# Kernel optimization log

Hardware: AMD Instinct MI355X
Metric: run time of the kernel (lower is better)

## Reference

```python
import jax, jax.numpy as jnp
import numpy as np
from jax import lax

H = 106      # hidden size
IN = 100     # input feature size
S = 512      # sequence length (time-major)
B = 256      # batch
N_REST = 10  # layers 2..6 of lstm1 (5) + all 5 layers of lstm2, all 106->106


def _lstm_layer(x, Wih, Whh, bih, bhh):
    """Single LSTM layer, PyTorch gate order (i, f, g, o). x: (S, B, in)."""
    # Precompute input contribution for all timesteps at once: (S, B, 4H)
    gx = jnp.einsum('sbi,gi->sbg', x, Wih) + bih + bhh

    def step(carry, g_t):
        h, c = carry
        g = g_t + h @ Whh.T                      # (B, 4H)
        i, f, gg, o = jnp.split(g, 4, axis=-1)
        i = jax.nn.sigmoid(i)
        f = jax.nn.sigmoid(f)
        gg = jnp.tanh(gg)
        o = jax.nn.sigmoid(o)
        c = f * c + i * gg
        h = o * jnp.tanh(c)
        return (h, c), h

    b = x.shape[1]
    h0 = jnp.zeros((b, H), x.dtype)
    c0 = jnp.zeros((b, H), x.dtype)
    _, ys = lax.scan(step, (h0, c0), gx)
    return ys  # (S, B, H)


def setup_inputs() -> dict:
    key = jax.random.key(0)
    ks = jax.random.split(key, 10)
    k = 1.0 / np.sqrt(H)  # PyTorch LSTM default uniform init bound
    u = lambda kk, shape: jax.random.uniform(kk, shape, jnp.float32, -k, k)

    noise = jax.random.normal(ks[0], (S, B, IN), jnp.float32)
    # First layer: input dim 100
    W_ih0 = u(ks[1], (4 * H, IN))
    W_hh0 = u(ks[2], (4 * H, H))
    b_ih0 = u(ks[3], (4 * H,))
    b_hh0 = u(ks[4], (4 * H,))
    # Remaining 10 layers: input dim 106, stacked
    W_ih = u(ks[5], (N_REST, 4 * H, H))
    W_hh = u(ks[6], (N_REST, 4 * H, H))
    b_ih = u(ks[7], (N_REST, 4 * H))
    b_hh = u(ks[8], (N_REST, 4 * H))
    return {"noise": noise, "W_ih0": W_ih0, "W_hh0": W_hh0, "b_ih0": b_ih0,
            "b_hh0": b_hh0, "W_ih": W_ih, "W_hh": W_hh, "b_ih": b_ih, "b_hh": b_hh}


def reference(noise, W_ih0, W_hh0, b_ih0, b_hh0, W_ih, W_hh, b_ih, b_hh):
    x = _lstm_layer(noise, W_ih0, W_hh0, b_ih0, b_hh0)

    def layer_step(xc, params):
        Wih, Whh, bih, bhh = params
        return _lstm_layer(xc, Wih, Whh, bih, bhh), None

    x, _ = lax.scan(layer_step, x, (W_ih, W_hh, b_ih, b_hh))
    return x  # (S, B, H)
```

## Files before the change

### kernel.cpp

```cpp
#include <hip/hip_runtime.h>
#include <cmath>


namespace {
constexpr int H = 106, G4 = 424, SEQ = 512, BB = 256, KIN0 = 100;
constexpr int GST = 436;
constexpr int NTHR = 896;
constexpr int RGN = 16;
constexpr int NLAYER = 11;
constexpr int RD = 16;
constexpr int REL = 56;
constexpr int KMAC = 8;
constexpr size_t CNT_STRIDE = 16;
constexpr size_t RING_OFF_B = 65536;
constexpr size_t RING_PER_L = (size_t)RD * BB * REL;

using f16x8 = __attribute__((ext_vector_type(8))) _Float16;
using f32x4 = __attribute__((ext_vector_type(4))) float;
typedef unsigned long long u64;

__device__ __forceinline__ u64 ald(const u64* p) {
    return __hip_atomic_load(p, __ATOMIC_RELAXED, __HIP_MEMORY_SCOPE_AGENT);
}
__device__ __forceinline__ void ast(u64* p, u64 v) {
    __hip_atomic_store(p, v, __ATOMIC_RELAXED, __HIP_MEMORY_SCOPE_AGENT);
}
__device__ __forceinline__ unsigned aldu(const unsigned* p) {
    return __hip_atomic_load(p, __ATOMIC_RELAXED, __HIP_MEMORY_SCOPE_AGENT);
}
__device__ __forceinline__ void astu(unsigned* p, unsigned v) {
    __hip_atomic_store(p, v, __ATOMIC_RELAXED, __HIP_MEMORY_SCOPE_AGENT);
}
__device__ __forceinline__ void spinc(const unsigned* p, unsigned tgt) {
    while (aldu(p) < tgt) __builtin_amdgcn_s_sleep(8);
}
__device__ __forceinline__ float fast_tanh(float x) {
    float t = __expf(2.0f * x);
    return 1.0f - 2.0f / (t + 1.0f);
}
__device__ __forceinline__ float act_gate(float g, bool istanh) {
    float s = istanh ? 2.0f * g : g;
    float r = 1.0f / (1.0f + __expf(-s));
    return istanh ? 2.0f * r - 1.0f : r;
}
__device__ __forceinline__ unsigned packh2(float a, float b) {
    unsigned lo = (unsigned)__builtin_bit_cast(unsigned short, (_Float16)a);
    unsigned hi = (unsigned)__builtin_bit_cast(unsigned short, (_Float16)b);
    return (hi << 16) | lo;
}

__global__ __launch_bounds__(NTHR)
__attribute__((amdgpu_waves_per_eu(4, 4)))
void lstm_wave(const float* __restrict__ noise,
               float* __restrict__ yout,
               unsigned* cnt, u64* ring,
               const float* __restrict__ W_ih0, const float* __restrict__ W_hh0,
               const float* __restrict__ b_ih0, const float* __restrict__ b_hh0,
               const float* __restrict__ W_ih,  const float* __restrict__ W_hh,
               const float* __restrict__ b_ih,  const float* __restrict__ b_hh)
{
    const int l = blockIdx.x / RGN;
    const int rg = blockIdx.x % RGN;
    const bool LAST = (l == NLAYER - 1);
    const int K_IN = (l == 0) ? KIN0 : H;

    const float* Wih = (l == 0) ? W_ih0 : W_ih + (size_t)(l - 1) * G4 * H;
    const float* Whh = (l == 0) ? W_hh0 : W_hh + (size_t)(l - 1) * G4 * H;
    const float* pbi = (l == 0) ? b_ih0 : b_ih + (size_t)(l - 1) * G4;
    const float* pbh = (l == 0) ? b_hh0 : b_hh + (size_t)(l - 1) * G4;

    unsigned* cons_my = cnt + (size_t)(l * RGN + rg) * CNT_STRIDE;
    unsigned* cons_in = cnt + (size_t)((l - 1) * RGN + rg) * CNT_STRIDE;
    u64* ring_in  = ring + (size_t)(l - 1) * RING_PER_L;
    u64* ring_out = ring + (size_t)l * RING_PER_L;

    __shared__ __align__(16) _Float16 sx[KMAC][16 * 136];
    __shared__ __align__(16) _Float16 sh[16 * 136];
    __shared__ float gl[16 * GST];

    const int tid = threadIdx.x;
    const int w = tid >> 6, lane = tid & 63;
    const int l16 = lane & 15, kg = lane >> 4;
    const int lm = tid / 56, ld = tid % 56;
    const int um = tid / 53, up = tid % 53;

    f16x8 bf[2][8];
    float bias[2];
    #pragma unroll
    for (int t = 0; t < 2; ++t) {
        const int n = 16 * (2 * w + t) + l16;
        const bool valid = n < G4;
        const float* pwx = Wih + (size_t)(valid ? n : 0) * K_IN;
        const float* pwh = Whh + (size_t)(valid ? n : 0) * H;
        #pragma unroll
        for (int q = 0; q < 8; ++q) {
            f16x8 v;
            #pragma unroll
            for (int e = 0; e < 8; ++e) {
                const int k = 32 * q + 8 * kg + e;
                float f = 0.0f;
                if (valid) {
                    if (k < 128) { if (k < K_IN) f = pwx[k]; }
                    else { const int kh = k - 128; if (kh < H) f = pwh[kh]; }
                }
                v[e] = (_Float16)f;
            }
            bf[t][q] = v;
        }
        bias[t] = valid ? (pbi[n] + pbh[n]) : 0.0f;
    }

    for (int i = tid; i < KMAC * 1088 + 1088; i += NTHR) {
        if (i < KMAC * 1088) ((unsigned*)sx)[i] = 0;
        else ((unsigned*)sh)[i - KMAC * 1088] = 0;
    }
    float c0 = 0.0f, c1 = 0.0f;
    __syncthreads();

    for (int m = 0; m < SEQ / KMAC; ++m) {
        unsigned xw[KMAC] = {0, 0, 0, 0, 0, 0, 0, 0};
        if (l == 0) {
            if (ld < 50) {
                #pragma unroll
                for (int ss = 0; ss < KMAC; ++ss) {
                    const int s = KMAC * m + ss;
                    const float2 t = *(const float2*)(noise +
                        ((size_t)s * BB + rg * 16 + lm) * KIN0 + 2 * ld);
                    xw[ss] = packh2(t.x, t.y);
                }
            }
        } else {
            u64 v[KMAC];
            #pragma unroll
            for (int ss = 0; ss < KMAC; ++ss) {
                const int s = KMAC * m + ss;
                v[ss] = ald(ring_in + ((size_t)(s & (RD - 1)) * BB + rg * 16 + lm) * REL + ld);
            }
            #pragma unroll
            for (int ss = 0; ss < KMAC; ++ss) {
                const int s = KMAC * m + ss;
                const unsigned expt = (unsigned)(s + 1);
                const u64* pin = ring_in + ((size_t)(s & (RD - 1)) * BB + rg * 16 + lm) * REL + ld;
                u64 vv = v[ss];
                while ((unsigned)(vv >> 32) != expt) { __builtin_amdgcn_s_sleep(2); vv = ald(pin); }
                xw[ss] = (unsigned)vv;
            }
        }
        if (tid == 0 && !LAST && m >= 2) spinc(cons_my, (unsigned)(KMAC * m - 8));
        if (l > 0 || ld < 50) {
            #pragma unroll
            for (int ss = 0; ss < KMAC; ++ss)
                ((unsigned*)sx)[ss * 1088 + lm * 68 + ld] = xw[ss];
        }
        __syncthreads();
        if (tid == 0 && l > 0) astu(cons_in, (unsigned)(KMAC * m + KMAC));

        for (int ss = 0; ss < KMAC; ++ss) {
            const int s = KMAC * m + ss;
            f32x4 acc[2] = {{0, 0, 0, 0}, {0, 0, 0, 0}};
            const _Float16* ax = &sx[ss][l16 * 136 + 8 * kg];
            #pragma unroll
            for (int q = 0; q < 4; ++q) {
                const f16x8 a = *(const f16x8*)(ax + 32 * q);
                acc[0] = __builtin_amdgcn_mfma_f32_16x16x32_f16(a, bf[0][q], acc[0], 0, 0, 0);
                acc[1] = __builtin_amdgcn_mfma_f32_16x16x32_f16(a, bf[1][q], acc[1], 0, 0, 0);
            }
            const _Float16* ah = &sh[l16 * 136 + 8 * kg];
            #pragma unroll
            for (int q = 4; q < 8; ++q) {
                const f16x8 a = *(const f16x8*)(ah + 32 * (q - 4));
                acc[0] = __builtin_amdgcn_mfma_f32_16x16x32_f16(a, bf[0][q], acc[0], 0, 0, 0);
                acc[1] = __builtin_amdgcn_mfma_f32_16x16x32_f16(a, bf[1][q], acc[1], 0, 0, 0);
            }
            #pragma unroll
            for (int t = 0; t < 2; ++t) {
                const int n = 16 * (2 * w + t) + l16;
                if (n < G4) {
                    const bool istanh = (n >= 2 * H) && (n < 3 * H);
                    #pragma unroll
                    for (int r = 0; r < 4; ++r)
                        gl[(4 * kg + r) * GST + n] = act_gate(acc[t][r] + bias[t], istanh);
                }
            }
            __syncthreads();

            if (tid < 848) {
                const float* gm = gl + um * GST;
                const float2 vi = *(const float2*)(gm + 2 * up);
                const float2 vf = *(const float2*)(gm + H + 2 * up);
                const float2 vg = *(const float2*)(gm + 2 * H + 2 * up);
                const float2 vo = *(const float2*)(gm + 3 * H + 2 * up);
                c0 = fmaf(vf.x, c0, vi.x * vg.x);
                c1 = fmaf(vf.y, c1, vi.y * vg.y);
                const float h0 = vo.x * fast_tanh(c0);
                const float h1 = vo.y * fast_tanh(c1);
                const unsigned hw = packh2(h0, h1);
                ((unsigned*)sh)[um * 68 + up] = hw;
                if (LAST) {
                    *(float2*)(yout + ((size_t)s * BB + rg * 16 + um) * H + 2 * up) =
                        make_float2(h0, h1);
                } else {
                    ast(ring_out + ((size_t)(s & (RD - 1)) * BB + rg * 16 + um) * REL + up,
                        ((u64)(unsigned)(s + 1) << 32) | hw);
                }
            } else if (!LAST) {
                const int t2 = tid - 848, mm = t2 / 3, dd = t2 % 3;
                ast(ring_out + ((size_t)(s & (RD - 1)) * BB + rg * 16 + mm) * REL + 53 + dd,
                    (u64)(unsigned)(s + 1) << 32);
            }
            __syncthreads();
        }
    }
}
}

extern "C" void kernel_launch(void* const* d_in, const int* in_sizes, int n_in,
                              void* d_out, int out_size, void* d_ws, size_t ws_size,
                              hipStream_t stream) {
    const float* noise = (const float*)d_in[0];
    const float* W_ih0 = (const float*)d_in[1];
    const float* W_hh0 = (const float*)d_in[2];
    const float* b_ih0 = (const float*)d_in[3];
    const float* b_hh0 = (const float*)d_in[4];
    const float* W_ih  = (const float*)d_in[5];
    const float* W_hh  = (const float*)d_in[6];
    const float* b_ih  = (const float*)d_in[7];
    const float* b_hh  = (const float*)d_in[8];

    const size_t clear_bytes = RING_OFF_B + (size_t)10 * RING_PER_L * sizeof(u64);
    hipMemsetAsync(d_ws, 0, clear_bytes, stream);

    unsigned* cnt = (unsigned*)d_ws;
    u64* ring = (u64*)((char*)d_ws + RING_OFF_B);

    lstm_wave<<<dim3(NLAYER * RGN), dim3(NTHR), 0, stream>>>(
        noise, (float*)d_out, cnt, ring,
        W_ih0, W_hh0, b_ih0, b_hh0, W_ih, W_hh, b_ih, b_hh);
}
```

Baseline: 1.287 ms.

## Shrink block to 8 waves and precompute next step's input MFMA off critical path

The block drops from 14 to 8 waves, so each wave now owns 3-4 gate column tiles instead of 2, and the elementwise and load work is looped twice per thread. The input-projection MFMAs for the next timestep are issued right after the cell update, before the barrier, so only the recurrent half stays on the serial per-step path. Fewer waves should make barriers cheaper. In exchange, each wave does more serial MFMA and elementwise work, and register pressure rises from holding 4 weight tiles plus the precomputed accumulators.

```diff
diff --git a/kernel.cpp b/kernel.cpp
--- a/kernel.cpp
+++ b/kernel.cpp
@@ -4,8 +4,8 @@
 
 namespace {
 constexpr int H = 106, G4 = 424, SEQ = 512, BB = 256, KIN0 = 100;
-constexpr int GST = 436;
-constexpr int NTHR = 896;
+constexpr int GST = 434;
+constexpr int NTHR = 512;
 constexpr int RGN = 16;
 constexpr int NLAYER = 11;
 constexpr int RD = 16;
@@ -50,7 +50,7 @@
 }
 
 __global__ __launch_bounds__(NTHR)
-__attribute__((amdgpu_waves_per_eu(4, 4)))
+__attribute__((amdgpu_waves_per_eu(2, 2)))
 void lstm_wave(const float* __restrict__ noise,
                float* __restrict__ yout,
                unsigned* cnt, u64* ring,
@@ -76,20 +76,20 @@
 
     __shared__ __align__(16) _Float16 sx[KMAC][16 * 136];
     __shared__ __align__(16) _Float16 sh[16 * 136];
-    __shared__ float gl[16 * GST];
+    __shared__ __align__(16) float gl[16 * GST];
 
     const int tid = threadIdx.x;
     const int w = tid >> 6, lane = tid & 63;
     const int l16 = lane & 15, kg = lane >> 4;
-    const int lm = tid / 56, ld = tid % 56;
-    const int um = tid / 53, up = tid % 53;
-
-    f16x8 bf[2][8];
-    float bias[2];
+    const int NT = (w < 4) ? 4 : 3;
+    const int tb = (w < 4) ? 4 * w : 16 + 3 * (w - 4);
+
+    f16x8 bf[4][8];
+    float bias[4];
     #pragma unroll
-    for (int t = 0; t < 2; ++t) {
-        const int n = 16 * (2 * w + t) + l16;
-        const bool valid = n < G4;
+    for (int t = 0; t < 4; ++t) {
+        const int n = 16 * (tb + t) + l16;
+        const bool valid = (t < NT) && (n < G4);
         const float* pwx = Wih + (size_t)(valid ? n : 0) * K_IN;
         const float* pwh = Whh + (size_t)(valid ? n : 0) * H;
         #pragma unroll
@@ -114,68 +114,90 @@
         if (i < KMAC * 1088) ((unsigned*)sx)[i] = 0;
         else ((unsigned*)sh)[i - KMAC * 1088] = 0;
     }
-    float c0 = 0.0f, c1 = 0.0f;
+    float c0[2] = {0.f, 0.f}, c1[2] = {0.f, 0.f};
     __syncthreads();
 
+    f32x4 accx[4];
+
     for (int m = 0; m < SEQ / KMAC; ++m) {
-        unsigned xw[KMAC] = {0, 0, 0, 0, 0, 0, 0, 0};
-        if (l == 0) {
-            if (ld < 50) {
-                #pragma unroll
-                for (int ss = 0; ss < KMAC; ++ss) {
-                    const int s = KMAC * m + ss;
-                    const float2 t = *(const float2*)(noise +
-                        ((size_t)s * BB + rg * 16 + lm) * KIN0 + 2 * ld);
-                    xw[ss] = packh2(t.x, t.y);
-                }
-            }
-        } else {
-            u64 v[KMAC];
-            #pragma unroll
-            for (int ss = 0; ss < KMAC; ++ss) {
-                const int s = KMAC * m + ss;
-                v[ss] = ald(ring_in + ((size_t)(s & (RD - 1)) * BB + rg * 16 + lm) * REL + ld);
-            }
-            #pragma unroll
-            for (int ss = 0; ss < KMAC; ++ss) {
-                const int s = KMAC * m + ss;
-                const unsigned expt = (unsigned)(s + 1);
-                const u64* pin = ring_in + ((size_t)(s & (RD - 1)) * BB + rg * 16 + lm) * REL + ld;
-                u64 vv = v[ss];
-                while ((unsigned)(vv >> 32) != expt) { __builtin_amdgcn_s_sleep(2); vv = ald(pin); }
-                xw[ss] = (unsigned)vv;
+        #pragma unroll
+        for (int e = 0; e < 2; ++e) {
+            const int flat = tid + NTHR * e;
+            if (flat < 896) {
+                const int lm = flat / 56, ld = flat % 56;
+                unsigned xw[KMAC];
+                if (l == 0) {
+                    #pragma unroll
+                    for (int ss = 0; ss < KMAC; ++ss) {
+                        unsigned r = 0;
+                        if (ld < 50) {
+                            const int s = KMAC * m + ss;
+                            const float2 t = *(const float2*)(noise +
+                                ((size_t)s * BB + rg * 16 + lm) * KIN0 + 2 * ld);
+                            r = packh2(t.x, t.y);
+                        }
+                        xw[ss] = r;
+                    }
+                } else {
+                    u64 v[KMAC];
+                    #pragma unroll
+                    for (int ss = 0; ss < KMAC; ++ss) {
+                        const int s = KMAC * m + ss;
+                        v[ss] = ald(ring_in + ((size_t)(s & (RD - 1)) * BB + rg * 16 + lm) * REL + ld);
+                    }
+                    #pragma unroll
+                    for (int ss = 0; ss < KMAC; ++ss) {
+                        const int s = KMAC * m + ss;
+                        const unsigned expt = (unsigned)(s + 1);
+                        const u64* pin = ring_in + ((size_t)(s & (RD - 1)) * BB + rg * 16 + lm) * REL + ld;
+                        u64 vv = v[ss];
+                        while ((unsigned)(vv >> 32) != expt) { __builtin_amdgcn_s_sleep(2); vv = ald(pin); }
+                        xw[ss] = (unsigned)vv;
+                    }
+                }
+                if (l > 0 || ld < 50) {
+                    #pragma unroll
+                    for (int ss = 0; ss < KMAC; ++ss)
+                        ((unsigned*)sx)[ss * 1088 + lm * 68 + ld] = xw[ss];
+                }
             }
         }
         if (tid == 0 && !LAST && m >= 2) spinc(cons_my, (unsigned)(KMAC * m - 8));
-        if (l > 0 || ld < 50) {
-            #pragma unroll
-            for (int ss = 0; ss < KMAC; ++ss)
-                ((unsigned*)sx)[ss * 1088 + lm * 68 + ld] = xw[ss];
-        }
         __syncthreads();
         if (tid == 0 && l > 0) astu(cons_in, (unsigned)(KMAC * m + KMAC));
 
+        {
+            #pragma unroll
+            for (int t = 0; t < 4; ++t) accx[t] = f32x4{0, 0, 0, 0};
+            const _Float16* ax = &sx[0][l16 * 136 + 8 * kg];
+            #pragma unroll
+            for (int q = 0; q < 4; ++q) {
+                const f16x8 a = *(const f16x8*)(ax + 32 * q);
+                #pragma unroll
+                for (int t = 0; t < 4; ++t)
+                    if (t < NT)
+                        accx[t] = __builtin_amdgcn_mfma_f32_16x16x32_f16(a, bf[t][q], accx[t], 0, 0, 0);
+            }
+        }
+
         for (int ss = 0; ss < KMAC; ++ss) {
             const int s = KMAC * m + ss;
-            f32x4 acc[2] = {{0, 0, 0, 0}, {0, 0, 0, 0}};
-            const _Float16* ax = &sx[ss][l16 * 136 + 8 * kg];
-            #pragma unroll
-            for (int q = 0; q < 4; ++q) {
-                const f16x8 a = *(const f16x8*)(ax + 32 * q);
-                acc[0] = __builtin_amdgcn_mfma_f32_16x16x32_f16(a, bf[0][q], acc[0], 0, 0, 0);
-                acc[1] = __builtin_amdgcn_mfma_f32_16x16x32_f16(a, bf[1][q], acc[1], 0, 0, 0);
-            }
+            f32x4 acc[4];
+            #pragma unroll
+            for (int t = 0; t < 4; ++t) acc[t] = accx[t];
             const _Float16* ah = &sh[l16 * 136 + 8 * kg];
             #pragma unroll
             for (int q = 4; q < 8; ++q) {
                 const f16x8 a = *(const f16x8*)(ah + 32 * (q - 4));
-                acc[0] = __builtin_amdgcn_mfma_f32_16x16x32_f16(a, bf[0][q], acc[0], 0, 0, 0);
-                acc[1] = __builtin_amdgcn_mfma_f32_16x16x32_f16(a, bf[1][q], acc[1], 0, 0, 0);
-            }
-            #pragma unroll
-            for (int t = 0; t < 2; ++t) {
-                const int n = 16 * (2 * w + t) + l16;
-                if (n < G4) {
+                #pragma unroll
+                for (int t = 0; t < 4; ++t)
+                    if (t < NT)
+                        acc[t] = __builtin_amdgcn_mfma_f32_16x16x32_f16(a, bf[t][q], acc[t], 0, 0, 0);
+            }
+            #pragma unroll
+            for (int t = 0; t < 4; ++t) {
+                const int n = 16 * (tb + t) + l16;
+                if (t < NT && n < G4) {
                     const bool istanh = (n >= 2 * H) && (n < 3 * H);
                     #pragma unroll
                     for (int r = 0; r < 4; ++r)
@@ -184,29 +206,47 @@
             }
             __syncthreads();
 
-            if (tid < 848) {
-                const float* gm = gl + um * GST;
-                const float2 vi = *(const float2*)(gm + 2 * up);
-                const float2 vf = *(const float2*)(gm + H + 2 * up);
-                const float2 vg = *(const float2*)(gm + 2 * H + 2 * up);
-                const float2 vo = *(const float2*)(gm + 3 * H + 2 * up);
-                c0 = fmaf(vf.x, c0, vi.x * vg.x);
-                c1 = fmaf(vf.y, c1, vi.y * vg.y);
-                const float h0 = vo.x * fast_tanh(c0);
-                const float h1 = vo.y * fast_tanh(c1);
-                const unsigned hw = packh2(h0, h1);
-                ((unsigned*)sh)[um * 68 + up] = hw;
-                if (LAST) {
-                    *(float2*)(yout + ((size_t)s * BB + rg * 16 + um) * H + 2 * up) =
-                        make_float2(h0, h1);
-                } else {
-                    ast(ring_out + ((size_t)(s & (RD - 1)) * BB + rg * 16 + um) * REL + up,
-                        ((u64)(unsigned)(s + 1) << 32) | hw);
-                }
-            } else if (!LAST) {
-                const int t2 = tid - 848, mm = t2 / 3, dd = t2 % 3;
-                ast(ring_out + ((size_t)(s & (RD - 1)) * BB + rg * 16 + mm) * REL + 53 + dd,
-                    (u64)(unsigned)(s + 1) << 32);
+            #pragma unroll
+            for (int e = 0; e < 2; ++e) {
+                const int item = tid + NTHR * e;
+                if (item < 848) {
+                    const int um = item / 53, up = item % 53;
+                    const float* gm = gl + um * GST;
+                    const float2 vi = *(const float2*)(gm + 2 * up);
+                    const float2 vf = *(const float2*)(gm + H + 2 * up);
+                    const float2 vg = *(const float2*)(gm + 2 * H + 2 * up);
+                    const float2 vo = *(const float2*)(gm + 3 * H + 2 * up);
+                    c0[e] = fmaf(vf.x, c0[e], vi.x * vg.x);
+                    c1[e] = fmaf(vf.y, c1[e], vi.y * vg.y);
+                    const float h0 = vo.x * fast_tanh(c0[e]);
+                    const float h1 = vo.y * fast_tanh(c1[e]);
+                    const unsigned hw = packh2(h0, h1);
+                    ((unsigned*)sh)[um * 68 + up] = hw;
+                    if (LAST) {
+                        *(float2*)(yout + ((size_t)s * BB + rg * 16 + um) * H + 2 * up) =
+                            make_float2(h0, h1);
+                    } else {
+                        ast(ring_out + ((size_t)(s & (RD - 1)) * BB + rg * 16 + um) * REL + up,
+                            ((u64)(unsigned)(s + 1) << 32) | hw);
+                    }
+                } else if (item < 896 && !LAST) {
+                    const int t2 = item - 848, mm = t2 / 3, dd = t2 % 3;
+                    ast(ring_out + ((size_t)(s & (RD - 1)) * BB + rg * 16 + mm) * REL + 53 + dd,
+                        (u64)(unsigned)(s + 1) << 32);
+                }
+            }
+            if (ss + 1 < KMAC) {
+                #pragma unroll
+                for (int t = 0; t < 4; ++t) accx[t] = f32x4{0, 0, 0, 0};
+                const _Float16* ax = &sx[ss + 1][l16 * 136 + 8 * kg];
+                #pragma unroll
+                for (int q = 0; q < 4; ++q) {
+                    const f16x8 a = *(const f16x8*)(ax + 32 * q);
+                    #pragma unroll
+                    for (int t = 0; t < 4; ++t)
+                        if (t < NT)
+                            accx[t] = __builtin_amdgcn_mfma_f32_16x16x32_f16(a, bf[t][q], accx[t], 0, 0, 0);
+                }
             }
             __syncthreads();
         }
```

Result: slower. 1.566 ms (+21.7%).

## Interleave two batch sub-tiles per block to overlap MFMA with gate updates

Applied to the files above, without the earlier changes.

Each block now owns two 16-row batch sub-tiles, with half as many blocks per layer. While one sub-tile runs its MFMA gate matmul, the other runs its elementwise cell/hidden update, so the two stages of the serial recurrence can overlap. The goal is to hide update and barrier latency per timestep. In exchange each block does twice the work and there are half as many blocks, the input chunk size is halved, and LDS use doubles.

```diff
diff --git a/kernel.cpp b/kernel.cpp
--- a/kernel.cpp
+++ b/kernel.cpp
@@ -6,11 +6,11 @@
 constexpr int H = 106, G4 = 424, SEQ = 512, BB = 256, KIN0 = 100;
 constexpr int GST = 436;
 constexpr int NTHR = 896;
-constexpr int RGN = 16;
+constexpr int RGN = 8;
 constexpr int NLAYER = 11;
 constexpr int RD = 16;
 constexpr int REL = 56;
-constexpr int KMAC = 8;
+constexpr int KMAC = 4;
 constexpr size_t CNT_STRIDE = 16;
 constexpr size_t RING_OFF_B = 65536;
 constexpr size_t RING_PER_L = (size_t)RD * BB * REL;
@@ -74,9 +74,9 @@
     u64* ring_in  = ring + (size_t)(l - 1) * RING_PER_L;
     u64* ring_out = ring + (size_t)l * RING_PER_L;
 
-    __shared__ __align__(16) _Float16 sx[KMAC][16 * 136];
-    __shared__ __align__(16) _Float16 sh[16 * 136];
-    __shared__ float gl[16 * GST];
+    __shared__ __align__(16) _Float16 sx[2][KMAC][16 * 136];
+    __shared__ __align__(16) _Float16 sh[2][16 * 136];
+    __shared__ float gl[2][16 * GST];
 
     const int tid = threadIdx.x;
     const int w = tid >> 6, lane = tid & 63;
@@ -110,107 +110,132 @@
         bias[t] = valid ? (pbi[n] + pbh[n]) : 0.0f;
     }
 
-    for (int i = tid; i < KMAC * 1088 + 1088; i += NTHR) {
-        if (i < KMAC * 1088) ((unsigned*)sx)[i] = 0;
-        else ((unsigned*)sh)[i - KMAC * 1088] = 0;
+    for (int i = tid; i < 2 * KMAC * 1088 + 2 * 1088; i += NTHR) {
+        if (i < 2 * KMAC * 1088) ((unsigned*)sx)[i] = 0;
+        else ((unsigned*)sh)[i - 2 * KMAC * 1088] = 0;
     }
-    float c0 = 0.0f, c1 = 0.0f;
+    float cA0 = 0.f, cA1 = 0.f, cB0 = 0.f, cB1 = 0.f;
     __syncthreads();
 
+    auto COMPUTE = [&](int st, int ss) {
+        f32x4 acc[2] = {{0, 0, 0, 0}, {0, 0, 0, 0}};
+        const _Float16* ax = &sx[st][ss][l16 * 136 + 8 * kg];
+        #pragma unroll
+        for (int q = 0; q < 4; ++q) {
+            const f16x8 a = *(const f16x8*)(ax + 32 * q);
+            acc[0] = __builtin_amdgcn_mfma_f32_16x16x32_f16(a, bf[0][q], acc[0], 0, 0, 0);
+            acc[1] = __builtin_amdgcn_mfma_f32_16x16x32_f16(a, bf[1][q], acc[1], 0, 0, 0);
+        }
+        const _Float16* ah = &sh[st][l16 * 136 + 8 * kg];
+        #pragma unroll
+        for (int q = 4; q < 8; ++q) {
+            const f16x8 a = *(const f16x8*)(ah + 32 * (q - 4));
+            acc[0] = __builtin_amdgcn_mfma_f32_16x16x32_f16(a, bf[0][q], acc[0], 0, 0, 0);
+            acc[1] = __builtin_amdgcn_mfma_f32_16x16x32_f16(a, bf[1][q], acc[1], 0, 0, 0);
+        }
+        #pragma unroll
+        for (int t = 0; t < 2; ++t) {
+            const int n = 16 * (2 * w + t) + l16;
+            if (n < G4) {
+                const bool istanh = (n >= 2 * H) && (n < 3 * H);
+                #pragma unroll
+                for (int r = 0; r < 4; ++r)
+                    gl[st][(4 * kg + r) * GST + n] = act_gate(acc[t][r] + bias[t], istanh);
+            }
+        }
+    };
+
+    auto UPDATE = [&](int st, int s, float& c0, float& c1) {
+        if (tid < 848) {
+            const float* gm = &gl[st][um * GST];
+            const float2 vi = *(const float2*)(gm + 2 * up);
+            const float2 vf = *(const float2*)(gm + H + 2 * up);
+            const float2 vg = *(const float2*)(gm + 2 * H + 2 * up);
+            const float2 vo = *(const float2*)(gm + 3 * H + 2 * up);
+            c0 = fmaf(vf.x, c0, vi.x * vg.x);
+            c1 = fmaf(vf.y, c1, vi.y * vg.y);
+            const float h0 = vo.x * fast_tanh(c0);
+            const float h1 = vo.y * fast_tanh(c1);
+            const unsigned hw = packh2(h0, h1);
+            ((unsigned*)&sh[st][0])[um * 68 + up] = hw;
+            const int grow = rg * 32 + st * 16 + um;
+            if (LAST) {
+                *(float2*)(yout + ((size_t)s * BB + grow) * H + 2 * up) =
+                    make_float2(h0, h1);
+            } else {
+                ast(ring_out + ((size_t)(s & (RD - 1)) * BB + grow) * REL + up,
+                    ((u64)(unsigned)(s + 1) << 32) | hw);
+            }
+        } else if (!LAST) {
+            const int t2 = tid - 848, mm = t2 / 3, dd = t2 % 3;
+            const int grow = rg * 32 + st * 16 + mm;
+            ast(ring_out + ((size_t)(s & (RD - 1)) * BB + grow) * REL + 53 + dd,
+                (u64)(unsigned)(s + 1) << 32);
+        }
+    };
+
     for (int m = 0; m < SEQ / KMAC; ++m) {
-        unsigned xw[KMAC] = {0, 0, 0, 0, 0, 0, 0, 0};
+        unsigned xw[2][KMAC];
         if (l == 0) {
-            if (ld < 50) {
+            #pragma unroll
+            for (int st = 0; st < 2; ++st)
+                #pragma unroll
+                for (int ss = 0; ss < KMAC; ++ss) {
+                    unsigned r = 0;
+                    if (ld < 50) {
+                        const int s = KMAC * m + ss;
+                        const int grow = rg * 32 + st * 16 + lm;
+                        const float2 t = *(const float2*)(noise +
+                            ((size_t)s * BB + grow) * KIN0 + 2 * ld);
+                        r = packh2(t.x, t.y);
+                    }
+                    xw[st][ss] = r;
+                }
+        } else {
+            u64 v[2][KMAC];
+            #pragma unroll
+            for (int st = 0; st < 2; ++st)
                 #pragma unroll
                 for (int ss = 0; ss < KMAC; ++ss) {
                     const int s = KMAC * m + ss;
-                    const float2 t = *(const float2*)(noise +
-                        ((size_t)s * BB + rg * 16 + lm) * KIN0 + 2 * ld);
-                    xw[ss] = packh2(t.x, t.y);
-                }
-            }
-        } else {
-            u64 v[KMAC];
-            #pragma unroll
-            for (int ss = 0; ss < KMAC; ++ss) {
-                const int s = KMAC * m + ss;
-                v[ss] = ald(ring_in + ((size_t)(s & (RD - 1)) * BB + rg * 16 + lm) * REL + ld);
-            }
-            #pragma unroll
-            for (int ss = 0; ss < KMAC; ++ss) {
-                const int s = KMAC * m + ss;
-                const unsigned expt = (unsigned)(s + 1);
-                const u64* pin = ring_in + ((size_t)(s & (RD - 1)) * BB + rg * 16 + lm) * REL + ld;
-                u64 vv = v[ss];
-                while ((unsigned)(vv >> 32) != expt) { __builtin_amdgcn_s_sleep(2); vv = ald(pin); }
-                xw[ss] = (unsigned)vv;
-            }
-        }
-        if (tid == 0 && !LAST && m >= 2) spinc(cons_my, (unsigned)(KMAC * m - 8));
+                    const int grow = rg * 32 + st * 16 + lm;
+                    v[st][ss] = ald(ring_in + ((size_t)(s & (RD - 1)) * BB + grow) * REL + ld);
+                }
+            #pragma unroll
+            for (int st = 0; st < 2; ++st)
+                #pragma unroll
+                for (int ss = 0; ss < KMAC; ++ss) {
+                    const int s = KMAC * m + ss;
+                    const unsigned expt = (unsigned)(s + 1);
+                    const int grow = rg * 32 + st * 16 + lm;
+                    const u64* pin = ring_in + ((size_t)(s & (RD - 1)) * BB + grow) * REL + ld;
+                    u64 vv = v[st][ss];
+                    while ((unsigned)(vv >> 32) != expt) { __builtin_amdgcn_s_sleep(2); vv = ald(pin); }
+                    xw[st][ss] = (unsigned)vv;
+                }
+        }
+        if (tid == 0 && !LAST && m >= 4) spinc(cons_my, (unsigned)(KMAC * m - 12));
         if (l > 0 || ld < 50) {
             #pragma unroll
-            for (int ss = 0; ss < KMAC; ++ss)
-                ((unsigned*)sx)[ss * 1088 + lm * 68 + ld] = xw[ss];
+            for (int st = 0; st < 2; ++st)
+                #pragma unroll
+                for (int ss = 0; ss < KMAC; ++ss)
+                    ((unsigned*)&sx[st][ss][0])[lm * 68 + ld] = xw[st][ss];
         }
         __syncthreads();
         if (tid == 0 && l > 0) astu(cons_in, (unsigned)(KMAC * m + KMAC));
 
         for (int ss = 0; ss < KMAC; ++ss) {
             const int s = KMAC * m + ss;
-            f32x4 acc[2] = {{0, 0, 0, 0}, {0, 0, 0, 0}};
-            const _Float16* ax = &sx[ss][l16 * 136 + 8 * kg];
-            #pragma unroll
-            for (int q = 0; q < 4; ++q) {
-                const f16x8 a = *(const f16x8*)(ax + 32 * q);
-                acc[0] = __builtin_amdgcn_mfma_f32_16x16x32_f16(a, bf[0][q], acc[0], 0, 0, 0);
-                acc[1] = __builtin_amdgcn_mfma_f32_16x16x32_f16(a, bf[1][q], acc[1], 0, 0, 0);
-            }
-            const _Float16* ah = &sh[l16 * 136 + 8 * kg];
-            #pragma unroll
-            for (int q = 4; q < 8; ++q) {
-                const f16x8 a = *(const f16x8*)(ah + 32 * (q - 4));
-                acc[0] = __builtin_amdgcn_mfma_f32_16x16x32_f16(a, bf[0][q], acc[0], 0, 0, 0);
-                acc[1] = __builtin_amdgcn_mfma_f32_16x16x32_f16(a, bf[1][q], acc[1], 0, 0, 0);
-            }
-            #pragma unroll
-            for (int t = 0; t < 2; ++t) {
-                const int n = 16 * (2 * w + t) + l16;
-                if (n < G4) {
-                    const bool istanh = (n >= 2 * H) && (n < 3 * H);
-                    #pragma unroll
-                    for (int r = 0; r < 4; ++r)
-                        gl[(4 * kg + r) * GST + n] = act_gate(acc[t][r] + bias[t], istanh);
-                }
-            }
+            COMPUTE(0, ss);
+            if (s > 0) UPDATE(1, s - 1, cB0, cB1);
             __syncthreads();
-
-            if (tid < 848) {
-                const float* gm = gl + um * GST;
-                const float2 vi = *(const float2*)(gm + 2 * up);
-                const float2 vf = *(const float2*)(gm + H + 2 * up);
-                const float2 vg = *(const float2*)(gm + 2 * H + 2 * up);
-                const float2 vo = *(const float2*)(gm + 3 * H + 2 * up);
-                c0 = fmaf(vf.x, c0, vi.x * vg.x);
-                c1 = fmaf(vf.y, c1, vi.y * vg.y);
-                const float h0 = vo.x * fast_tanh(c0);
-                const float h1 = vo.y * fast_tanh(c1);
-                const unsigned hw = packh2(h0, h1);
-                ((unsigned*)sh)[um * 68 + up] = hw;
-                if (LAST) {
-                    *(float2*)(yout + ((size_t)s * BB + rg * 16 + um) * H + 2 * up) =
-                        make_float2(h0, h1);
-                } else {
-                    ast(ring_out + ((size_t)(s & (RD - 1)) * BB + rg * 16 + um) * REL + up,
-                        ((u64)(unsigned)(s + 1) << 32) | hw);
-                }
-            } else if (!LAST) {
-                const int t2 = tid - 848, mm = t2 / 3, dd = t2 % 3;
-                ast(ring_out + ((size_t)(s & (RD - 1)) * BB + rg * 16 + mm) * REL + 53 + dd,
-                    (u64)(unsigned)(s + 1) << 32);
-            }
+            COMPUTE(1, ss);
+            UPDATE(0, s, cA0, cA1);
             __syncthreads();
         }
     }
+    UPDATE(1, SEQ - 1, cB0, cB1);
 }
 }
 
```

Result: slower. 2.435 ms (+89.2%).
